# Kernel tuning notes

Hardware: AMD Instinct MI355X
Metric: run time of the kernel (lower is better)

The kernel has to match this reference:

```python
import jax, jax.numpy as jnp
import numpy as np

NUM_CODES = 512
LATENT_DIM = 256
B, C, H, W = 64, 256, 32, 32


def setup_inputs() -> dict:
    key = jax.random.key(0)
    k1, k2 = jax.random.split(key)
    z = jax.random.normal(k1, (B, C, H, W), dtype=jnp.float32)
    # nn.Embedding init: uniform(-1/num_codes, 1/num_codes)
    codebook = jax.random.uniform(
        k2, (NUM_CODES, LATENT_DIM), dtype=jnp.float32,
        minval=-1.0 / NUM_CODES, maxval=1.0 / NUM_CODES)
    return {"z": z, "codebook": codebook}


def reference(z, codebook):
    b, c, h, w = z.shape
    # [B, HW, C]
    z_flat = z.reshape(b, c, h * w).transpose(0, 2, 1)
    # squared L2 distances via ||z||^2 - 2 z.e + ||e||^2 -> [B, HW, K]
    distances = (
        jnp.sum(z_flat ** 2, axis=-1, keepdims=True)
        - 2.0 * jnp.einsum('bnc,kc->bnk', z_flat, codebook)
        + jnp.sum(codebook ** 2, axis=-1)
    )
    encoding_indices = jnp.argmin(distances, axis=-1)  # [B, HW]
    # gather -> [B, HW, C] -> permute -> [B, C, HW] -> reshape to z.shape
    z_q = codebook[encoding_indices].transpose(0, 2, 1).reshape(z.shape)
    return z_q, encoding_indices
```

## Files before the change

### kernel.cpp

```cpp
#include <hip/hip_runtime.h>
#include <hip/hip_bf16.h>

#define K_CODES 512
#define CDIM    256
#define HW      1024
#define NBATCH  64
#define SZ      260

typedef float  f32x16 __attribute__((ext_vector_type(16)));
typedef short  bf16x8 __attribute__((ext_vector_type(8)));

__device__ __forceinline__ unsigned short f2bf(float x) {
    unsigned u = __float_as_uint(x);
    unsigned r = (u + 0x7FFFu + ((u >> 16) & 1u)) >> 16;
    return (unsigned short)r;
}

__global__ __launch_bounds__(64) void vq_prep(const float* __restrict__ cb,
                                              float* __restrict__ enorm,
                                              unsigned short* __restrict__ cb16) {
    int k = blockIdx.x;
    int l = threadIdx.x;
    float4 v = *reinterpret_cast<const float4*>(cb + (size_t)k * CDIM + l * 4);
    float s = (v.x * v.x + v.y * v.y) + (v.z * v.z + v.w * v.w);
#pragma unroll
    for (int off = 1; off < 64; off <<= 1) s += __shfl_xor(s, off, 64);
    if (l == 0) enorm[k] = s;
    ushort4 o;
    o.x = f2bf(v.x); o.y = f2bf(v.y); o.z = f2bf(v.z); o.w = f2bf(v.w);
    *reinterpret_cast<ushort4*>(cb16 + (size_t)k * CDIM + l * 4) = o;
}

__global__ __launch_bounds__(64) void vq_enorm(const float* __restrict__ cb,
                                               float* __restrict__ enorm) {
    int k = blockIdx.x;
    int l = threadIdx.x;
    float4 v = *reinterpret_cast<const float4*>(cb + (size_t)k * CDIM + l * 4);
    float s = (v.x * v.x + v.y * v.y) + (v.z * v.z + v.w * v.w);
#pragma unroll
    for (int off = 1; off < 64; off <<= 1) s += __shfl_xor(s, off, 64);
    if (l == 0) enorm[k] = s;
}

__global__ __launch_bounds__(512) void vq_pass1(const float* __restrict__ z,
                                                const unsigned short* __restrict__ cb16,
                                                unsigned* __restrict__ cnt_out,
                                                unsigned short* __restrict__ codes_out,
                                                int* __restrict__ idx_out) {
    __shared__ __align__(16) unsigned short zs[256 * 256];
    __shared__ __align__(16) unsigned short es[32 * 256];
    __shared__ unsigned       cnt_lds[256];
    __shared__ __align__(16) unsigned short codes_lds[256 * 16];

    const int t = threadIdx.x;
    const int l = t & 63, w = t >> 6;
    const int r0 = blockIdx.x << 8;
    const int b  = r0 >> 10, n0 = r0 & 1023;
    const float* zb = z + (size_t)b * (CDIM * HW);

    if (t < 256) cnt_lds[t] = 0;

    unsigned* zsw = (unsigned*)zs;
#pragma unroll
    for (int p = 0; p < 16; ++p) {
        int c2 = (p << 3) + w;
        int iq = l;
        const float* g0 = zb + (size_t)(2 * c2) * HW + n0 + (iq << 2);
        float4 a  = *reinterpret_cast<const float4*>(g0);
        float4 bb = *reinterpret_cast<const float4*>(g0 + HW);
        int up = (((c2 >> 2) ^ (iq & 7)) << 2) + (c2 & 3);
        const float* ap = &a.x; const float* bp = &bb.x;
#pragma unroll
        for (int j = 0; j < 4; ++j) {
            unsigned pk = (unsigned)f2bf(ap[j]) | ((unsigned)f2bf(bp[j]) << 16);
            zsw[((iq << 2) + j) * 128 + up] = pk;
        }
    }
    __syncthreads();

    const int lrow = l & 31, lh = l >> 5;
    const int lf = (lrow >> 2) & 7;
    const int row = (w << 5) + lrow;
    bf16x8 zf[16];
#pragma unroll
    for (int s = 0; s < 16; ++s) {
        int u = (2 * s + lh) ^ lf;
        zf[s] = *reinterpret_cast<const bf16x8*>(&zs[row * 256 + (u << 3)]);
    }

    float sa = 0.f;
#pragma unroll
    for (int s = 0; s < 16; ++s)
#pragma unroll
        for (int j = 0; j < 8; ++j)
            sa += fabsf(__uint_as_float(((unsigned)(unsigned short)zf[s][j]) << 16));
    sa += __shfl_xor(sa, 32, 64);

    float g_lane = -3.4e38f;
    for (int r = 0; r < 16; ++r) {
        __syncthreads();
#pragma unroll
        for (int q = 0; q < 2; ++q) {
            int lin  = (q << 9) + t;
            int code = lin >> 5, u = lin & 31;
            uint4 v = *reinterpret_cast<const uint4*>(&cb16[(size_t)((r << 5) + code) * 256 + (u << 3)]);
            *reinterpret_cast<uint4*>(&es[code * 256 + ((u ^ ((code >> 2) & 7)) << 3)]) = v;
        }
        __syncthreads();

        f32x16 accA = {0.f,0.f,0.f,0.f,0.f,0.f,0.f,0.f,0.f,0.f,0.f,0.f,0.f,0.f,0.f,0.f};
        f32x16 accB = accA;
#pragma unroll
        for (int s = 0; s < 16; s += 2) {
            int uA = (2 * s + lh) ^ lf;
            int uB = (2 * s + 2 + lh) ^ lf;
            bf16x8 a0 = *reinterpret_cast<const bf16x8*>(&es[lrow * 256 + (uA << 3)]);
            bf16x8 a1 = *reinterpret_cast<const bf16x8*>(&es[lrow * 256 + (uB << 3)]);
            accA = __builtin_amdgcn_mfma_f32_32x32x16_bf16(a0, zf[s],     accA, 0, 0, 0);
            accB = __builtin_amdgcn_mfma_f32_32x32x16_bf16(a1, zf[s + 1], accB, 0, 0, 0);
        }
#pragma unroll
        for (int i = 0; i < 16; ++i) g_lane = fmaxf(g_lane, accA[i] + accB[i]);
    }
    float g = fmaxf(g_lane, __shfl_xor(g_lane, 32, 64));
    const float thr = g - (sa * 1.7e-5f + 6.0e-4f);

    for (int r = 0; r < 16; ++r) {
        __syncthreads();
#pragma unroll
        for (int q = 0; q < 2; ++q) {
            int lin  = (q << 9) + t;
            int code = lin >> 5, u = lin & 31;
            uint4 v = *reinterpret_cast<const uint4*>(&cb16[(size_t)((r << 5) + code) * 256 + (u << 3)]);
            *reinterpret_cast<uint4*>(&es[code * 256 + ((u ^ ((code >> 2) & 7)) << 3)]) = v;
        }
        __syncthreads();

        f32x16 accA = {0.f,0.f,0.f,0.f,0.f,0.f,0.f,0.f,0.f,0.f,0.f,0.f,0.f,0.f,0.f,0.f};
        f32x16 accB = accA;
#pragma unroll
        for (int s = 0; s < 16; s += 2) {
            int uA = (2 * s + lh) ^ lf;
            int uB = (2 * s + 2 + lh) ^ lf;
            bf16x8 a0 = *reinterpret_cast<const bf16x8*>(&es[lrow * 256 + (uA << 3)]);
            bf16x8 a1 = *reinterpret_cast<const bf16x8*>(&es[lrow * 256 + (uB << 3)]);
            accA = __builtin_amdgcn_mfma_f32_32x32x16_bf16(a0, zf[s],     accA, 0, 0, 0);
            accB = __builtin_amdgcn_mfma_f32_32x32x16_bf16(a1, zf[s + 1], accB, 0, 0, 0);
        }
#pragma unroll
        for (int i = 0; i < 16; ++i) {
            float v = accA[i] + accB[i];
            if (v >= thr) {
                int code = (r << 5) + (i & 3) + 8 * (i >> 2) + 4 * lh;
                unsigned pos = atomicAdd(&cnt_lds[row], 1u);
                if (pos < 16) codes_lds[row * 16 + pos] = (unsigned short)code;
            }
        }
    }
    __syncthreads();

    if (t < 256) {
        unsigned c = cnt_lds[t];
        cnt_out[r0 + t] = c;
        if (c == 1) idx_out[r0 + t] = (int)codes_lds[t * 16];
        uint4* src = reinterpret_cast<uint4*>(&codes_lds[t * 16]);
        uint4* dst = reinterpret_cast<uint4*>(&codes_out[(size_t)(r0 + t) * 16]);
        dst[0] = src[0]; dst[1] = src[1];
    }
}

__global__ __launch_bounds__(256) void vq_rescore(const float* __restrict__ z,
                                                  const float* __restrict__ cb,
                                                  const float* __restrict__ enb,
                                                  const unsigned* __restrict__ cnt_in,
                                                  const unsigned short* __restrict__ codes_in,
                                                  int* __restrict__ idx_out) {
    __shared__ __align__(16) float zst[32 * 256];
    __shared__ float znl[32];
    __shared__ unsigned cntl[32];
    __shared__ unsigned short rows2[32];
    __shared__ int nr2;

    const int t  = threadIdx.x;
    const int r0 = blockIdx.x << 5;
    const int b  = r0 >> 10, n0 = r0 & 1023;
    const float* zb = z + (size_t)b * (CDIM * HW);

#pragma unroll
    for (int p = 0; p < 8; ++p) {
        int c  = (p << 5) + (t >> 3);
        int i0 = (t & 7) << 2;
        float4 v = *reinterpret_cast<const float4*>(zb + (size_t)c * HW + n0 + i0);
        int u = c >> 2, c3 = c & 3;
        const float* vp = &v.x;
#pragma unroll
        for (int j = 0; j < 4; ++j) {
            int rw = i0 + j;
            zst[rw * 256 + ((u ^ ((rw >> 2) & 7)) << 2) + c3] = vp[j];
        }
    }
    if (t == 0) nr2 = 0;
    __syncthreads();

    if (t < 32) {
        float s0 = 0.f, s1 = 0.f, s2 = 0.f, s3 = 0.f;
        int f = (t >> 2) & 7;
        for (int u = 0; u < 64; ++u) {
            float4 v = *reinterpret_cast<const float4*>(&zst[t * 256 + ((u ^ f) << 2)]);
            s0 += v.x * v.x; s1 += v.y * v.y; s2 += v.z * v.z; s3 += v.w * v.w;
        }
        znl[t] = (s0 + s1) + (s2 + s3);
        unsigned c = cnt_in[r0 + t];
        cntl[t] = c;
        if (c != 1u) {
            int p = atomicAdd(&nr2, 1);
            rows2[p] = (unsigned short)t;
        }
    }
    __syncthreads();

    const int w = t >> 6, lane = t & 63;
    const int slot = lane >> 4, j = lane & 15;
    const int n2 = nr2;

    for (int base = w * 4; base < n2; base += 16) {
        int ri = base + slot;
        bool active = (ri < n2);
        int row_l = active ? (int)rows2[ri] : 0;
        unsigned cr = cntl[row_l];
        const float* zp = &zst[row_l * 256];
        const int f = (row_l >> 2) & 7;
        const float zn = znl[row_l];
        unsigned long long pk = 0xFFFFFFFFFFFFFFFFull;

        if (cr <= 16u) {
            if (active && j < (int)cr) {
                int code = (int)codes_in[(size_t)(r0 + row_l) * 16 + j];
                const float* ep = cb + (size_t)code * CDIM;
                float acc = 0.f;
                for (int u = 0; u < 64; ++u) {
                    float4 zv = *reinterpret_cast<const float4*>(&zp[(u ^ f) << 2]);
                    float4 ev = *reinterpret_cast<const float4*>(ep + (u << 2));
                    acc += zv.x * ev.x;
                    acc += zv.y * ev.y;
                    acc += zv.z * ev.z;
                    acc += zv.w * ev.w;
                }
                float d = (zn - 2.0f * acc) + enb[code];
                pk = (((unsigned long long)__float_as_uint(d)) << 32) | (unsigned)code;
            }
        } else if (active) {
            for (int b2 = 0; b2 < 32; ++b2) {
                int code = (b2 << 4) + j;
                const float* ep = cb + (size_t)code * CDIM;
                float acc = 0.f;
                for (int u = 0; u < 64; ++u) {
                    float4 zv = *reinterpret_cast<const float4*>(&zp[(u ^ f) << 2]);
                    float4 ev = *reinterpret_cast<const float4*>(ep + (u << 2));
                    acc += zv.x * ev.x; acc += zv.y * ev.y;
                    acc += zv.z * ev.z; acc += zv.w * ev.w;
                }
                float d = (zn - 2.0f * acc) + enb[code];
                unsigned long long q2 =
                    (((unsigned long long)__float_as_uint(d)) << 32) | (unsigned)code;
                if (q2 < pk) pk = q2;
            }
        }
#pragma unroll
        for (int o = 1; o < 16; o <<= 1) {
            unsigned long long q2 = __shfl_xor(pk, o, 64);
            if (q2 < pk) pk = q2;
        }
        if (active && j == 0)
            idx_out[r0 + row_l] = (int)(unsigned)(pk & 0xFFFFFFFFu);
    }
}

__global__ __launch_bounds__(512) void vq_argmin(const float* __restrict__ z,
                                                 const float* __restrict__ cb,
                                                 const float* __restrict__ enorm,
                                                 int* __restrict__ out_idx) {
    __shared__ float zs[64][SZ];
    __shared__ float es[64][SZ];
    __shared__ float ens[K_CODES];
    __shared__ float zn[64];
    __shared__ float red_d[64][32];
    __shared__ int   red_i[64][32];

    const int t  = threadIdx.x;
    const int r0 = blockIdx.x * 64;
    const int b  = r0 >> 10;
    const int n0 = r0 & 1023;
    const float* zb = z + (size_t)b * CDIM * HW;

#pragma unroll
    for (int p = 0; p < 8; ++p) {
        int lin = p * 512 + t;
        int c   = lin >> 4;
        int i0  = (lin & 15) << 2;
        float4 v = *reinterpret_cast<const float4*>(zb + (size_t)c * HW + n0 + i0);
        zs[i0 + 0][c] = v.x; zs[i0 + 1][c] = v.y;
        zs[i0 + 2][c] = v.z; zs[i0 + 3][c] = v.w;
    }
    if (t < K_CODES) ens[t] = enorm[t];
    __syncthreads();

    if (t < 64) {
        float s0 = 0.f, s1 = 0.f, s2 = 0.f, s3 = 0.f;
        for (int c = 0; c < CDIM; c += 4) {
            float4 v = *reinterpret_cast<const float4*>(&zs[t][c]);
            s0 += v.x * v.x; s1 += v.y * v.y; s2 += v.z * v.z; s3 += v.w * v.w;
        }
        zn[t] = (s0 + s1) + (s2 + s3);
    }

    const int ty = t >> 5, tx = t & 31, row0 = ty * 4;
    float best_d[4]; int best_i[4];
#pragma unroll
    for (int i = 0; i < 4; ++i) { best_d[i] = 3.4e38f; best_i[i] = 0; }

    for (int K0 = 0; K0 < K_CODES; K0 += 64) {
        __syncthreads();
#pragma unroll
        for (int p = 0; p < 8; ++p) {
            int lin = p * 512 + t;
            int j = lin >> 6, c4 = (lin & 63) << 2;
            *reinterpret_cast<float4*>(&es[j][c4]) =
                *reinterpret_cast<const float4*>(cb + (size_t)(K0 + j) * CDIM + c4);
        }
        __syncthreads();

        float acc[4][2];
#pragma unroll
        for (int i = 0; i < 4; ++i) { acc[i][0] = 0.f; acc[i][1] = 0.f; }
#pragma unroll 4
        for (int k = 0; k < CDIM; k += 4) {
            float4 a0 = *reinterpret_cast<const float4*>(&zs[row0 + 0][k]);
            float4 a1 = *reinterpret_cast<const float4*>(&zs[row0 + 1][k]);
            float4 a2 = *reinterpret_cast<const float4*>(&zs[row0 + 2][k]);
            float4 a3 = *reinterpret_cast<const float4*>(&zs[row0 + 3][k]);
            float4 e0 = *reinterpret_cast<const float4*>(&es[tx][k]);
            float4 e1 = *reinterpret_cast<const float4*>(&es[tx + 32][k]);
            float4 aa[4] = {a0, a1, a2, a3};
#pragma unroll
            for (int i = 0; i < 4; ++i) {
#pragma unroll
                for (int j = 0; j < 2; ++j) {
                    float4 e = j ? e1 : e0;
                    acc[i][j] += aa[i].x * e.x; acc[i][j] += aa[i].y * e.y;
                    acc[i][j] += aa[i].z * e.z; acc[i][j] += aa[i].w * e.w;
                }
            }
        }
#pragma unroll
        for (int i = 0; i < 4; ++i) {
            float zni = zn[row0 + i];
#pragma unroll
            for (int j = 0; j < 2; ++j) {
                int code = K0 + j * 32 + tx;
                float d = (zni - 2.0f * acc[i][j]) + ens[code];
                if (d < best_d[i]) { best_d[i] = d; best_i[i] = code; }
            }
        }
    }
    __syncthreads();
#pragma unroll
    for (int i = 0; i < 4; ++i) {
        red_d[row0 + i][tx] = best_d[i];
        red_i[row0 + i][tx] = best_i[i];
    }
    __syncthreads();
    if (t < 64) {
        float bd = red_d[t][0]; int bi = red_i[t][0];
        for (int x = 1; x < 32; ++x) {
            float d = red_d[t][x]; int ii = red_i[t][x];
            if (d < bd || (d == bd && ii < bi)) { bd = d; bi = ii; }
        }
        out_idx[r0 + t] = bi;
    }
}

__global__ __launch_bounds__(256) void vq_gather(const float* __restrict__ cb,
                                                 const int* __restrict__ idx,
                                                 float* __restrict__ out) {
    const int blk = blockIdx.x;
    const int b   = blk >> 4;
    const int n0  = (blk & 15) << 6;
    const int t   = threadIdx.x;
    const int n   = t & 63;
    const int c0  = t >> 6;
    const int code = idx[b * HW + n0 + n];
    const float* crow = cb + (size_t)code * CDIM;
    float* ob = out + (size_t)b * CDIM * HW + n0 + n;

    if (c0 == 0)
        out[(size_t)NBATCH * CDIM * HW + (size_t)b * HW + n0 + n] = (float)code;

#pragma unroll 4
    for (int q = 0; q < 64; q += 4) {
        int c = c0 * 64 + q;
        float4 v = *reinterpret_cast<const float4*>(crow + c);
        ob[(size_t)(c + 0) * HW] = v.x;
        ob[(size_t)(c + 1) * HW] = v.y;
        ob[(size_t)(c + 2) * HW] = v.z;
        ob[(size_t)(c + 3) * HW] = v.w;
    }
}

extern "C" void kernel_launch(void* const* d_in, const int* in_sizes, int n_in,
                              void* d_out, int out_size, void* d_ws, size_t ws_size,
                              hipStream_t stream) {
    const float* z  = (const float*)d_in[0];
    const float* cb = (const float*)d_in[1];
    float* out = (float*)d_out;

    int*            idx   = (int*)d_ws;
    float*          en    = (float*)((char*)d_ws + 262144);
    unsigned short* cb16  = (unsigned short*)((char*)d_ws + 264192);
    unsigned*       cnt   = (unsigned*)((char*)d_ws + 526336);
    unsigned short* codes = (unsigned short*)((char*)d_ws + 788480);
    const size_t NEED_FULL = 2885632;

    if (ws_size >= NEED_FULL) {
        vq_prep   <<<dim3(K_CODES), dim3(64),  0, stream>>>(cb, en, cb16);
        vq_pass1  <<<dim3(256),     dim3(512), 0, stream>>>(z, cb16, cnt, codes, idx);
        vq_rescore<<<dim3(2048),    dim3(256), 0, stream>>>(z, cb, en, cnt, codes, idx);
    } else {
        vq_enorm  <<<dim3(K_CODES), dim3(64),  0, stream>>>(cb, en);
        vq_argmin <<<dim3(1024),    dim3(512), 0, stream>>>(z, cb, en, idx);
    }
    vq_gather<<<dim3(1024), dim3(256), 0, stream>>>(cb, idx, out);
}
```

Baseline: 126.6 us.

## Make VQ pass1 single-pass with running-max candidate filtering and double-buffered codebook

Replaces the two full sweeps over the codebook (one to find the max dot product, one to emit candidates) with a single sweep. It keeps a running max, emits candidates against a slightly looser padded threshold, and filters them afterwards against the final threshold using stored values. Codebook tiles are prefetched into registers and double-buffered in LDS using a rotation swizzle. Blocks are halved to 128 rows and 256 threads with two blocks per CU, reusing the z staging memory for codebook buffers. The risk is candidate overflow from the looser early threshold, which forces more rows into the rescore fallback.

```diff
diff --git a/kernel.cpp b/kernel.cpp
--- a/kernel.cpp
+++ b/kernel.cpp
@@ -42,29 +42,48 @@
     if (l == 0) enorm[k] = s;
 }
 
-__global__ __launch_bounds__(512) void vq_pass1(const float* __restrict__ z,
-                                                const unsigned short* __restrict__ cb16,
-                                                unsigned* __restrict__ cnt_out,
-                                                unsigned short* __restrict__ codes_out,
-                                                int* __restrict__ idx_out) {
-    __shared__ __align__(16) unsigned short zs[256 * 256];
-    __shared__ __align__(16) unsigned short es[32 * 256];
-    __shared__ unsigned       cnt_lds[256];
-    __shared__ __align__(16) unsigned short codes_lds[256 * 16];
+#define LOADPH(ph, R) do {                                                              \
+    int c0p = ((ph) & 15) << 5;                                                         \
+    _Pragma("unroll")                                                                   \
+    for (int q = 0; q < 4; ++q) {                                                       \
+        int li = (q << 8) + t; int cd = li >> 5; int uu = li & 31;                      \
+        int uo = (uu - cd) & 31;                                                        \
+        R[q] = *reinterpret_cast<const uint4*>(cb16 + (size_t)((c0p + cd) << 8) + (uo << 3)); \
+    } } while (0)
+
+#define STOREPH(bsel, R) do {                                                           \
+    unsigned short* eb_ = es + ((bsel) ? 8192 : 0);                                     \
+    _Pragma("unroll")                                                                   \
+    for (int q = 0; q < 4; ++q) {                                                       \
+        int li = (q << 8) + t;                                                          \
+        *reinterpret_cast<uint4*>(eb_ + (li << 3)) = R[q];                              \
+    } } while (0)
+
+__global__ __launch_bounds__(256, 2) void vq_pass1(const float* __restrict__ z,
+                                                   const unsigned short* __restrict__ cb16,
+                                                   unsigned* __restrict__ cnt_out,
+                                                   unsigned short* __restrict__ codes_out,
+                                                   int* __restrict__ idx_out) {
+    __shared__ __align__(16) char smem[65536];
+    unsigned short* zs    = (unsigned short*)smem;
+    unsigned*       zsw   = (unsigned*)smem;
+    unsigned short* es    = (unsigned short*)smem;
+    unsigned*       cntl  = (unsigned*)(smem + 32768);
+    float*          thrl  = (float*)(smem + 33280);
+    float*          valsl = (float*)(smem + 33792);
+    unsigned short* codesl= (unsigned short*)(smem + 41984);
 
     const int t = threadIdx.x;
     const int l = t & 63, w = t >> 6;
-    const int r0 = blockIdx.x << 8;
+    const int r0 = blockIdx.x << 7;
     const int b  = r0 >> 10, n0 = r0 & 1023;
     const float* zb = z + (size_t)b * (CDIM * HW);
 
-    if (t < 256) cnt_lds[t] = 0;
-
-    unsigned* zsw = (unsigned*)zs;
 #pragma unroll
     for (int p = 0; p < 16; ++p) {
-        int c2 = (p << 3) + w;
-        int iq = l;
+        int lin = (p << 8) + t;
+        int c2  = lin >> 5;
+        int iq  = lin & 31;
         const float* g0 = zb + (size_t)(2 * c2) * HW + n0 + (iq << 2);
         float4 a  = *reinterpret_cast<const float4*>(g0);
         float4 bb = *reinterpret_cast<const float4*>(g0 + HW);
@@ -79,7 +98,7 @@
     __syncthreads();
 
     const int lrow = l & 31, lh = l >> 5;
-    const int lf = (lrow >> 2) & 7;
+    const int lf  = (lrow >> 2) & 7;
     const int row = (w << 5) + lrow;
     bf16x8 zf[16];
 #pragma unroll
@@ -87,7 +106,6 @@
         int u = (2 * s + lh) ^ lf;
         zf[s] = *reinterpret_cast<const bf16x8*>(&zs[row * 256 + (u << 3)]);
     }
-
     float sa = 0.f;
 #pragma unroll
     for (int s = 0; s < 16; ++s)
@@ -96,76 +114,82 @@
             sa += fabsf(__uint_as_float(((unsigned)(unsigned short)zf[s][j]) << 16));
     sa += __shfl_xor(sa, 32, 64);
 
-    float g_lane = -3.4e38f;
-    for (int r = 0; r < 16; ++r) {
+    __syncthreads();
+
+    if (t < 128) cntl[t] = 0;
+    uint4 Ra[4], Rb[4];
+    LOADPH(0, Ra); LOADPH(1, Rb);
+    STOREPH(0, Ra);
+    __syncthreads();
+
+    const float pad_emit = sa * 1.8e-5f + 7.5e-4f;
+    float runmax = -3.4e38f;
+
+    for (int p = 0; p < 18; ++p) {
+        if (p < 17) { if ((p & 1) == 0) STOREPH(1, Rb); else STOREPH(0, Ra); }
+        if (p < 16) { if ((p & 1) == 0) LOADPH(p + 2, Ra); else LOADPH(p + 2, Rb); }
         __syncthreads();
-#pragma unroll
-        for (int q = 0; q < 2; ++q) {
-            int lin  = (q << 9) + t;
-            int code = lin >> 5, u = lin & 31;
-            uint4 v = *reinterpret_cast<const uint4*>(&cb16[(size_t)((r << 5) + code) * 256 + (u << 3)]);
-            *reinterpret_cast<uint4*>(&es[code * 256 + ((u ^ ((code >> 2) & 7)) << 3)]) = v;
-        }
-        __syncthreads();
+
+        const unsigned short* eb = es + ((p & 1) ? 8192 : 0);
+        const int code0 = (p & 15) << 5;
 
         f32x16 accA = {0.f,0.f,0.f,0.f,0.f,0.f,0.f,0.f,0.f,0.f,0.f,0.f,0.f,0.f,0.f,0.f};
         f32x16 accB = accA;
 #pragma unroll
         for (int s = 0; s < 16; s += 2) {
-            int uA = (2 * s + lh) ^ lf;
-            int uB = (2 * s + 2 + lh) ^ lf;
-            bf16x8 a0 = *reinterpret_cast<const bf16x8*>(&es[lrow * 256 + (uA << 3)]);
-            bf16x8 a1 = *reinterpret_cast<const bf16x8*>(&es[lrow * 256 + (uB << 3)]);
+            int u0 = (2 * s + lh + lrow) & 31;
+            int u1 = (2 * s + 2 + lh + lrow) & 31;
+            bf16x8 a0 = *reinterpret_cast<const bf16x8*>(&eb[(lrow << 8) + (u0 << 3)]);
+            bf16x8 a1 = *reinterpret_cast<const bf16x8*>(&eb[(lrow << 8) + (u1 << 3)]);
             accA = __builtin_amdgcn_mfma_f32_32x32x16_bf16(a0, zf[s],     accA, 0, 0, 0);
             accB = __builtin_amdgcn_mfma_f32_32x32x16_bf16(a1, zf[s + 1], accB, 0, 0, 0);
         }
-#pragma unroll
-        for (int i = 0; i < 16; ++i) g_lane = fmaxf(g_lane, accA[i] + accB[i]);
-    }
-    float g = fmaxf(g_lane, __shfl_xor(g_lane, 32, 64));
-    const float thr = g - (sa * 1.7e-5f + 6.0e-4f);
-
-    for (int r = 0; r < 16; ++r) {
+
+        float bm = -3.4e38f;
+        float v[16];
+#pragma unroll
+        for (int i = 0; i < 16; ++i) { v[i] = accA[i] + accB[i]; bm = fmaxf(bm, v[i]); }
+
+        if (p >= 2) {
+            float thr_e = runmax - pad_emit;
+#pragma unroll
+            for (int i = 0; i < 16; ++i) {
+                if (v[i] >= thr_e) {
+                    int code = code0 + (i & 3) + 8 * (i >> 2) + 4 * lh;
+                    unsigned pos = atomicAdd(&cntl[row], 1u);
+                    if (pos < 16u) {
+                        valsl[row * 16 + pos]  = v[i];
+                        codesl[row * 16 + pos] = (unsigned short)code;
+                    }
+                }
+            }
+        }
+        bm = fmaxf(bm, __shfl_xor(bm, 32, 64));
+        runmax = fmaxf(runmax, bm);
         __syncthreads();
-#pragma unroll
-        for (int q = 0; q < 2; ++q) {
-            int lin  = (q << 9) + t;
-            int code = lin >> 5, u = lin & 31;
-            uint4 v = *reinterpret_cast<const uint4*>(&cb16[(size_t)((r << 5) + code) * 256 + (u << 3)]);
-            *reinterpret_cast<uint4*>(&es[code * 256 + ((u ^ ((code >> 2) & 7)) << 3)]) = v;
-        }
-        __syncthreads();
-
-        f32x16 accA = {0.f,0.f,0.f,0.f,0.f,0.f,0.f,0.f,0.f,0.f,0.f,0.f,0.f,0.f,0.f,0.f};
-        f32x16 accB = accA;
-#pragma unroll
-        for (int s = 0; s < 16; s += 2) {
-            int uA = (2 * s + lh) ^ lf;
-            int uB = (2 * s + 2 + lh) ^ lf;
-            bf16x8 a0 = *reinterpret_cast<const bf16x8*>(&es[lrow * 256 + (uA << 3)]);
-            bf16x8 a1 = *reinterpret_cast<const bf16x8*>(&es[lrow * 256 + (uB << 3)]);
-            accA = __builtin_amdgcn_mfma_f32_32x32x16_bf16(a0, zf[s],     accA, 0, 0, 0);
-            accB = __builtin_amdgcn_mfma_f32_32x32x16_bf16(a1, zf[s + 1], accB, 0, 0, 0);
-        }
-#pragma unroll
-        for (int i = 0; i < 16; ++i) {
-            float v = accA[i] + accB[i];
-            if (v >= thr) {
-                int code = (r << 5) + (i & 3) + 8 * (i >> 2) + 4 * lh;
-                unsigned pos = atomicAdd(&cnt_lds[row], 1u);
-                if (pos < 16) codes_lds[row * 16 + pos] = (unsigned short)code;
-            }
-        }
-    }
-    __syncthreads();
-
-    if (t < 256) {
-        unsigned c = cnt_lds[t];
-        cnt_out[r0 + t] = c;
-        if (c == 1) idx_out[r0 + t] = (int)codes_lds[t * 16];
-        uint4* src = reinterpret_cast<uint4*>(&codes_lds[t * 16]);
-        uint4* dst = reinterpret_cast<uint4*>(&codes_out[(size_t)(r0 + t) * 16]);
-        dst[0] = src[0]; dst[1] = src[1];
+    }
+
+    if (lh == 0) thrl[row] = runmax - (sa * 1.7e-5f + 6.0e-4f);
+    __syncthreads();
+
+    if (t < 128) {
+        unsigned raw = cntl[t];
+        if (raw > 16u) {
+            cnt_out[r0 + t] = 17u;
+        } else {
+            float tf = thrl[t];
+            int kept = 0; unsigned short last = 0;
+            for (unsigned e = 0; e < raw; ++e) {
+                float vv = valsl[t * 16 + e];
+                if (vv >= tf) {
+                    unsigned short cc = codesl[t * 16 + e];
+                    codes_out[(size_t)(r0 + t) * 16 + kept] = cc;
+                    last = cc; ++kept;
+                }
+            }
+            cnt_out[r0 + t] = (unsigned)kept;
+            if (kept == 1) idx_out[r0 + t] = (int)last;
+        }
     }
 }
 
@@ -423,7 +447,7 @@
 
     if (ws_size >= NEED_FULL) {
         vq_prep   <<<dim3(K_CODES), dim3(64),  0, stream>>>(cb, en, cb16);
-        vq_pass1  <<<dim3(256),     dim3(512), 0, stream>>>(z, cb16, cnt, codes, idx);
+        vq_pass1  <<<dim3(512),     dim3(256), 0, stream>>>(z, cb16, cnt, codes, idx);
         vq_rescore<<<dim3(2048),    dim3(256), 0, stream>>>(z, cb, en, cnt, codes, idx);
     } else {
         vq_enorm  <<<dim3(K_CODES), dim3(64),  0, stream>>>(cb, en);
```

Result: slower. 245.6 us (+93.9%).
